# Performance work log

Measured on AMD Instinct MI355X. Metric: run time of the kernel, lower is better.

Reference implementation:

```python
import jax, jax.numpy as jnp
import numpy as np
from jax import lax

VOCAB, EMB, HID, TAGS = 8000, 300, 512, 24  # hidden_dim=512 -> 256 per direction
B, S = 128, 512
H2 = HID // 2


def setup_inputs() -> dict:
    key = jax.random.key(0)
    ks = jax.random.split(key, 16)
    sc = 0.05
    inp = {
        "chars": jax.random.randint(ks[0], (B, S), 0, VOCAB),
        "tags": jax.random.randint(ks[1], (B, S), 0, TAGS),
        "mask": jnp.ones((B, S), dtype=bool),
        "emb": jax.random.normal(ks[2], (VOCAB, EMB), jnp.float32) * sc,
        # PyTorch LSTM layout: gates stacked [i, f, g, o]
        "w_ih_f": jax.random.normal(ks[3], (4 * H2, EMB), jnp.float32) * sc,
        "w_hh_f": jax.random.normal(ks[4], (4 * H2, H2), jnp.float32) * sc,
        "b_f": jax.random.normal(ks[5], (4 * H2,), jnp.float32) * sc,  # b_ih + b_hh fused
        "w_ih_b": jax.random.normal(ks[6], (4 * H2, EMB), jnp.float32) * sc,
        "w_hh_b": jax.random.normal(ks[7], (4 * H2, H2), jnp.float32) * sc,
        "b_b": jax.random.normal(ks[8], (4 * H2,), jnp.float32) * sc,
        "w_out": jax.random.normal(ks[9], (TAGS, HID), jnp.float32) * sc,
        "b_out": jax.random.normal(ks[10], (TAGS,), jnp.float32) * sc,
        "trans": jax.random.normal(ks[11], (TAGS, TAGS), jnp.float32) * sc,
        "start_trans": jax.random.normal(ks[12], (TAGS,), jnp.float32) * sc,
        "end_trans": jax.random.normal(ks[13], (TAGS,), jnp.float32) * sc,
    }
    return inp


def _lstm_dir(x, w_ih, w_hh, b, reverse):
    # x: [B, S, E] -> h: [B, S, H2]
    gx = jnp.einsum('bse,ge->bsg', x, w_ih) + b  # [B, S, 4*H2]

    def step(carry, g_t):
        h, c = carry
        g = g_t + h @ w_hh.T
        i, f, gg, o = jnp.split(g, 4, axis=-1)
        c = jax.nn.sigmoid(f) * c + jax.nn.sigmoid(i) * jnp.tanh(gg)
        h = jax.nn.sigmoid(o) * jnp.tanh(c)
        return (h, c), h

    init = (jnp.zeros((x.shape[0], H2), x.dtype), jnp.zeros((x.shape[0], H2), x.dtype))
    _, hs = lax.scan(step, init, jnp.swapaxes(gx, 0, 1), reverse=reverse)
    return jnp.swapaxes(hs, 0, 1)


def _crf_loss(emissions, tags, mask, trans, start_trans, end_trans):
    # torchcrf log-likelihood, reduction='mean'; loss = -mean
    b, s, t = emissions.shape
    maskf = mask.astype(emissions.dtype)
    # numerator: score of gold path
    em_t = jnp.take_along_axis(emissions, tags[..., None], axis=2)[..., 0]  # [B,S]
    tr_t = trans[tags[:, :-1], tags[:, 1:]]  # [B,S-1]
    score = start_trans[tags[:, 0]] + em_t[:, 0]
    score = score + jnp.sum((em_t[:, 1:] + tr_t) * maskf[:, 1:], axis=1)
    seq_ends = jnp.sum(mask.astype(jnp.int32), axis=1) - 1  # [B]
    last_tags = jnp.take_along_axis(tags, seq_ends[:, None], axis=1)[:, 0]
    score = score + end_trans[last_tags]
    # denominator: forward algorithm via scan
    alpha0 = start_trans + emissions[:, 0]  # [B,T]

    def step(alpha, inputs):
        em, m = inputs  # em [B,T], m [B]
        nxt = jax.nn.logsumexp(alpha[:, :, None] + trans[None] + em[:, None, :], axis=1)
        alpha = jnp.where(m[:, None], nxt, alpha)
        return alpha, None

    alpha, _ = lax.scan(step, alpha0,
                        (jnp.swapaxes(emissions[:, 1:], 0, 1), jnp.swapaxes(mask[:, 1:], 0, 1)))
    log_z = jax.nn.logsumexp(alpha + end_trans, axis=1)  # [B]
    llh = score - log_z
    return -jnp.mean(llh)


def reference(chars, tags, mask, emb, w_ih_f, w_hh_f, b_f, w_ih_b, w_hh_b, b_b,
              w_out, b_out, trans, start_trans, end_trans):
    x = emb[chars]  # [B,S,E]
    h_f = _lstm_dir(x, w_ih_f, w_hh_f, b_f, reverse=False)
    h_b = _lstm_dir(x, w_ih_b, w_hh_b, b_b, reverse=True)
    lstm_out = jnp.concatenate([h_f, h_b], axis=-1)  # [B,S,HID]
    emissions = jnp.einsum('bsh,th->bst', lstm_out, w_out) + b_out  # [B,S,TAGS]
    return _crf_loss(emissions, tags, mask, trans, start_trans, end_trans)
```

## Files before the change

### kernel.cpp

```cpp
#include <hip/hip_runtime.h>
#include <math.h>

#define BB   128
#define SS   512
#define EMBD 300
#define VOC  8000
#define NTAG 24
#define BSD  (BB*SS)

#define RQI  36
#define LQQ  7

#define SW   400.0f
#define SH   512.0f
#define INVQ (1.0f / (400.0f * 512.0f))

typedef unsigned int   u32;
typedef unsigned short u16;
typedef _Float16 f16x2 __attribute__((ext_vector_type(2)));

__device__ __forceinline__ int idot4(u32 a, u32 b, int c) {
#if __has_builtin(__builtin_amdgcn_sdot4)
    return __builtin_amdgcn_sdot4((int)a, (int)b, c, false);
#elif __has_builtin(__builtin_amdgcn_sudot4)
    return __builtin_amdgcn_sudot4(true, (int)a, true, (int)b, c, false);
#else
    int s = c;
    #pragma unroll
    for (int e = 0; e < 4; ++e) {
        int xa = ((int)(a << (24 - 8 * e))) >> 24;
        int xb = ((int)(b << (24 - 8 * e))) >> 24;
        s += xa * xb;
    }
    return s;
#endif
}
__device__ __forceinline__ float sigm(float x) { return 1.0f / (1.0f + __expf(-x)); }
__device__ __forceinline__ float tanh_fast(float x) {
    return 1.0f - 2.0f / (__expf(2.0f * x) + 1.0f);
}
__device__ __forceinline__ int qclamp(float x, float s) {
    int v = (int)rintf(x * s);
    return v > 127 ? 127 : (v < -127 ? -127 : v);
}
__device__ __forceinline__ u32 q4(const float* p, float s) {
    u32 r = 0;
    #pragma unroll
    for (int e = 0; e < 4; ++e)
        r |= ((u32)(qclamp(p[e], s) & 0xFF)) << (8 * e);
    return r;
}

__global__ __launch_bounds__(512)
void k_packW(const float* __restrict__ w_hh_f, const float* __restrict__ w_hh_b,
             const float* __restrict__ w_out,
             u32* __restrict__ wregB, uint4* __restrict__ wldsB,
             u32* __restrict__ woq)
{
    const int dir = blockIdx.x;
    const int t   = threadIdx.x;
    const float* w = dir ? w_hh_b : w_hh_f;

    for (int half = 0; half < 2; ++half) {
        const int r = half * 512 + t;
        const float* row = w + (size_t)r * 256;
        for (int q = 0; q < RQI; ++q)
            wregB[((size_t)(dir * 2 + half) * RQI + q) * 512 + t] = q4(row + 4 * q, SW);
        for (int qq = 0; qq < LQQ; ++qq) {
            uint4 v;
            v.x = q4(row + 4 * (RQI + 4 * qq + 0), SW);
            v.y = q4(row + 4 * (RQI + 4 * qq + 1), SW);
            v.z = q4(row + 4 * (RQI + 4 * qq + 2), SW);
            v.w = q4(row + 4 * (RQI + 4 * qq + 3), SW);
            wldsB[((size_t)(dir * 2 + half) * LQQ + qq) * 512 + t] = v;
        }
    }
    for (int i = t; i < NTAG * 64; i += 512) {
        const int tag = i >> 6, q = i & 63;
        woq[(size_t)dir * NTAG * 64 + i] =
            q4(w_out + (size_t)tag * 512 + dir * 256 + 4 * q, SW);
    }
}

__global__ __launch_bounds__(256)
void k_gxtab(const float* __restrict__ emb,
             const float* __restrict__ w_f, const float* __restrict__ bias_f,
             const float* __restrict__ w_b, const float* __restrict__ bias_b,
             u16* __restrict__ gxtab)
{
    const int dir = blockIdx.z;
    const float* W    = dir ? w_b    : w_f;
    const float* bias = dir ? bias_b : bias_f;
    u16* out = gxtab + (size_t)dir * VOC * 1024;
    const int r0 = blockIdx.y * 64;
    const int c0 = blockIdx.x * 128;

    __shared__ float As[16][65];
    __shared__ float Bs[16][129];

    const int tid = threadIdx.x;
    const int kk = tid & 15;
    const int rr = tid >> 4;
    const int ty = tid >> 4;
    const int tx = tid & 15;

    float acc[4][8] = {};

    for (int kt = 0; kt < EMBD; kt += 16) {
        const int k = kt + kk;
        const bool kok = (k < EMBD);
        #pragma unroll
        for (int p = 0; p < 4; ++p)
            As[kk][rr + p * 16] = kok ? emb[(size_t)(r0 + rr + p * 16) * EMBD + k] : 0.0f;
        #pragma unroll
        for (int p = 0; p < 8; ++p)
            Bs[kk][rr + p * 16] = kok ? W[(size_t)(c0 + rr + p * 16) * EMBD + k] : 0.0f;
        __syncthreads();
        #pragma unroll
        for (int q = 0; q < 16; ++q) {
            float av[4], bv[8];
            #pragma unroll
            for (int i = 0; i < 4; ++i) av[i] = As[q][ty * 4 + i];
            #pragma unroll
            for (int jj = 0; jj < 8; ++jj) bv[jj] = Bs[q][jj * 16 + tx];
            #pragma unroll
            for (int i = 0; i < 4; ++i)
                #pragma unroll
                for (int jj = 0; jj < 8; ++jj)
                    acc[i][jj] = fmaf(av[i], bv[jj], acc[i][jj]);
        }
        __syncthreads();
    }

    #pragma unroll
    for (int i = 0; i < 4; ++i) {
        const size_t rb = (size_t)(r0 + ty * 4 + i) * 1024;
        #pragma unroll
        for (int jj = 0; jj < 8; ++jj) {
            const int cl = c0 + jj * 16 + tx;
            out[rb + cl] = __builtin_bit_cast(u16, (_Float16)(acc[i][jj] + bias[cl]));
        }
    }
}

__global__ __launch_bounds__(512, 2)
void k_lstm_res(const int* __restrict__ chars, const u16* __restrict__ gxtab,
                const u32* __restrict__ wregB, const uint4* __restrict__ wldsB,
                const u32* __restrict__ woq, const float* __restrict__ b_out,
                float* __restrict__ emis_f, float* __restrict__ emis_b)
{
    const int bid = blockIdx.x;
    const int dir = bid >> 7;
    const int b   = bid & 127;
    const int tid = threadIdx.x;

    __shared__ __align__(16) uint4 ldsW[2 * LQQ * 512];
    __shared__ __align__(16) u32   hq[2][64];
    __shared__ __align__(16) u32   woL[NTAG * 64];
    __shared__ __align__(16) float2 xg[256];
    __shared__ int chlds[SS];

    chlds[tid] = chars[(size_t)b * SS + tid];
    const uint4* wl = wldsB + (size_t)dir * 2 * LQQ * 512;
    #pragma unroll
    for (int q = 0; q < 2 * LQQ; ++q) ldsW[q * 512 + tid] = wl[(size_t)q * 512 + tid];
    {
        const u32* wop = woq + (size_t)dir * NTAG * 64;
        for (int i = tid; i < NTAG * 64; i += 512) woL[i] = wop[i];
    }
    if (tid < 64) hq[0][tid] = 0u;

    u32 WA[RQI], WB[RQI];
    const u32* wr = wregB + (size_t)dir * 2 * RQI * 512 + tid;
    #pragma unroll
    for (int q = 0; q < RQI; ++q) {
        WA[q] = wr[(size_t)q * 512];
        WB[q] = wr[(size_t)(RQI + q) * 512];
    }

    const u16* gxp = gxtab + (size_t)dir * VOC * 1024;
    float* emis = (dir ? emis_b : emis_f) + (size_t)b * SS * NTAG;

    const int tag = tid >> 4, part = tid & 15;
    const float bo = (tid < 384 && dir == 0) ? b_out[tag] : 0.0f;

    float c = 0.0f;
    __syncthreads();

    const int t0 = dir ? (SS - 1) : 0;
    u16 gA = gxp[(size_t)chlds[t0] * 1024 + tid];
    u16 gB = gxp[(size_t)chlds[t0] * 1024 + 512 + tid];

    int cur = 0;
    #pragma unroll 1
    for (int sloc = 0; sloc < SS; ++sloc) {
        const int t = dir ? (SS - 1 - sloc) : sloc;

        u16 gA_n = 0, gB_n = 0;
        if (sloc < SS - 1) {
            const int tn = dir ? (t - 1) : (t + 1);
            const size_t o = (size_t)chlds[tn] * 1024 + tid;
            gA_n = gxp[o];
            gB_n = gxp[o + 512];
        }

        const uint4* h16 = (const uint4*)hq[cur];
        int aA = 0, aB = 0;
        #pragma unroll
        for (int q16 = 0; q16 < 9; ++q16) {
            const uint4 hv = h16[q16];
            aA = idot4(WA[4 * q16 + 0], hv.x, aA);
            aA = idot4(WA[4 * q16 + 1], hv.y, aA);
            aA = idot4(WA[4 * q16 + 2], hv.z, aA);
            aA = idot4(WA[4 * q16 + 3], hv.w, aA);
            aB = idot4(WB[4 * q16 + 0], hv.x, aB);
            aB = idot4(WB[4 * q16 + 1], hv.y, aB);
            aB = idot4(WB[4 * q16 + 2], hv.z, aB);
            aB = idot4(WB[4 * q16 + 3], hv.w, aB);
        }
        #pragma unroll
        for (int qq = 0; qq < LQQ; ++qq) {
            const uint4 hv = h16[9 + qq];
            const uint4 wa = ldsW[qq * 512 + tid];
            const uint4 wb = ldsW[(LQQ + qq) * 512 + tid];
            aA = idot4(wa.x, hv.x, aA);
            aA = idot4(wa.y, hv.y, aA);
            aA = idot4(wa.z, hv.z, aA);
            aA = idot4(wa.w, hv.w, aA);
            aB = idot4(wb.x, hv.x, aB);
            aB = idot4(wb.y, hv.y, aB);
            aB = idot4(wb.z, hv.z, aB);
            aB = idot4(wb.w, hv.w, aB);
        }
        const float apreA = (float)aA * INVQ + (float)__builtin_bit_cast(_Float16, gA);
        const float apreB = (float)aB * INVQ + (float)__builtin_bit_cast(_Float16, gB);

        if (tid >= 256) xg[tid - 256] = make_float2(sigm(apreA), sigm(apreB));
        __syncthreads();

        if (tid < 256) {
            const float2 fo = xg[tid];
            const float ig = sigm(apreA);
            const float gg = tanh_fast(apreB);
            c = fmaf(fo.x, c, ig * gg);
            const float h = fo.y * tanh_fast(c);
            const int hi = qclamp(h, SH);
            const int b1 = __shfl_down(hi, 1);
            const int b2 = __shfl_down(hi, 2);
            const int b3 = __shfl_down(hi, 3);
            if ((tid & 3) == 0)
                hq[cur ^ 1][tid >> 2] = (u32)(hi & 0xFF) | ((u32)(b1 & 0xFF) << 8) |
                                        ((u32)(b2 & 0xFF) << 16) | ((u32)(b3 & 0xFF) << 24);
        }
        __syncthreads();

        if (tid < 384) {
            const uint4 hv = ((const uint4*)hq[cur ^ 1])[part];
            const uint4 wv = ((const uint4*)woL)[tag * 16 + part];
            int ei = idot4(wv.x, hv.x, 0);
            ei = idot4(wv.y, hv.y, ei);
            ei = idot4(wv.z, hv.z, ei);
            ei = idot4(wv.w, hv.w, ei);
            float e = (float)ei * INVQ;
            e += __shfl_down(e, 8);
            e += __shfl_down(e, 4);
            e += __shfl_down(e, 2);
            e += __shfl_down(e, 1);
            if (part == 0) emis[(size_t)t * NTAG + tag] = e + bo;
        }
        gA = gA_n; gB = gB_n;
        cur ^= 1;
    }
}

__global__ __launch_bounds__(64)
void k_crf(const float* __restrict__ emis_f, const float* __restrict__ emis_b,
           const int* __restrict__ tags,
           const float* __restrict__ trans, const float* __restrict__ start_tr,
           const float* __restrict__ end_tr, float* __restrict__ llh)
{
    const int b    = blockIdx.x;
    const int lane = threadIdx.x;
    const float* ef = emis_f + (size_t)b * SS * NTAG;
    const float* eb = emis_b + (size_t)b * SS * NTAG;
    const int*   tg = tags + (size_t)b * SS;
    const bool active = (lane < NTAG);

    float trans_reg[NTAG];
    #pragma unroll
    for (int i = 0; i < NTAG; ++i)
        trans_reg[i] = active ? trans[i * NTAG + lane] : 0.0f;

    float sc = 0.0f;
    for (int t = lane; t < SS; t += 64) {
        const int tt = tg[t];
        sc += ef[t * NTAG + tt] + eb[t * NTAG + tt];
        if (t > 0) sc += trans[tg[t - 1] * NTAG + tt];
    }
    #pragma unroll
    for (int off = 32; off > 0; off >>= 1) sc += __shfl_down(sc, off);

    float alpha = active ? (start_tr[lane] + ef[lane] + eb[lane]) : -1e30f;
    for (int t = 1; t < SS; ++t) {
        float v[NTAG];
        #pragma unroll
        for (int i = 0; i < NTAG; ++i)
            v[i] = __shfl(alpha, i) + trans_reg[i];
        float m = v[0];
        #pragma unroll
        for (int i = 1; i < NTAG; ++i) m = fmaxf(m, v[i]);
        float ssum = 0.0f;
        #pragma unroll
        for (int i = 0; i < NTAG; ++i) ssum += __expf(v[i] - m);
        const float e = active ? (ef[t * NTAG + lane] + eb[t * NTAG + lane]) : 0.0f;
        alpha = active ? (m + __logf(ssum) + e) : -1e30f;
    }

    float v = alpha + (active ? end_tr[lane] : 0.0f);
    float m = v;
    #pragma unroll
    for (int off = 32; off > 0; off >>= 1) m = fmaxf(m, __shfl_down(m, off));
    m = __shfl(m, 0);
    float e = __expf(v - m);
    #pragma unroll
    for (int off = 32; off > 0; off >>= 1) e += __shfl_down(e, off);

    if (lane == 0) {
        const float logz  = m + __logf(e);
        const float score = sc + start_tr[tg[0]] + end_tr[tg[SS - 1]];
        llh[b] = score - logz;
    }
}

__global__ __launch_bounds__(64)
void k_final(const float* __restrict__ llh, float* __restrict__ out)
{
    const int lane = threadIdx.x;
    float v = llh[lane] + llh[lane + 64];
    #pragma unroll
    for (int off = 32; off > 0; off >>= 1) v += __shfl_down(v, off);
    if (lane == 0) out[0] = -(v * (1.0f / 128.0f));
}

extern "C" void kernel_launch(void* const* d_in, const int* in_sizes, int n_in,
                              void* d_out, int out_size, void* d_ws, size_t ws_size,
                              hipStream_t stream)
{
    (void)in_sizes; (void)n_in; (void)out_size; (void)ws_size;

    const int*   chars   = (const int*)d_in[0];
    const int*   tags    = (const int*)d_in[1];
    const float* emb     = (const float*)d_in[3];
    const float* w_ih_f  = (const float*)d_in[4];
    const float* w_hh_f  = (const float*)d_in[5];
    const float* b_f     = (const float*)d_in[6];
    const float* w_ih_b  = (const float*)d_in[7];
    const float* w_hh_b  = (const float*)d_in[8];
    const float* b_b     = (const float*)d_in[9];
    const float* w_out   = (const float*)d_in[10];
    const float* b_out   = (const float*)d_in[11];
    const float* trans   = (const float*)d_in[12];
    const float* start_t = (const float*)d_in[13];
    const float* end_t   = (const float*)d_in[14];

    char* ws = (char*)d_ws;
    size_t off = 0;
    auto carve = [&](size_t bytes) -> char* {
        char* p = ws + off;
        off += (bytes + 255) & ~(size_t)255;
        return p;
    };
    u16*   gxtab  = (u16*)carve((size_t)2 * VOC * 1024 * 2);
    u32*   wregB  = (u32*)carve((size_t)2 * 2 * RQI * 512 * 4);
    uint4* wldsB  = (uint4*)carve((size_t)2 * 2 * LQQ * 512 * 16);
    u32*   woq    = (u32*)carve((size_t)2 * NTAG * 64 * 4);
    float* emis_f = (float*)carve((size_t)BSD * NTAG * 4);
    float* emis_b = (float*)carve((size_t)BSD * NTAG * 4);
    float* llh    = (float*)carve(128 * 4);

    hipLaunchKernelGGL(k_packW, dim3(2), dim3(512), 0, stream,
                       w_hh_f, w_hh_b, w_out, wregB, wldsB, woq);
    hipLaunchKernelGGL(k_gxtab, dim3(8, 125, 2), dim3(256), 0, stream,
                       emb, w_ih_f, b_f, w_ih_b, b_b, gxtab);
    hipLaunchKernelGGL(k_lstm_res, dim3(256), dim3(512), 0, stream,
                       chars, gxtab, wregB, wldsB, woq, b_out, emis_f, emis_b);
    hipLaunchKernelGGL(k_crf, dim3(128), dim3(64), 0, stream,
                       emis_f, emis_b, tags, trans, start_t, end_t, llh);
    hipLaunchKernelGGL(k_final, dim3(1), dim3(64), 0, stream,
                       llh, (float*)d_out);
}
```

Before: 1.203 ms.

## Broadcast hidden state via readlane and split recurrent weights across registers, LDS, global

The recurrent LSTM kernel now keeps the packed int8 hidden state in a per-lane register and broadcasts each word with readlane instead of reading uint4 vectors from LDS every step. The recurrent weight matrix is re-split three ways: 32 words per thread in registers (fewer than the previous 72), 14 uint4 per thread in LDS, and 10 uint4 per thread streamed from global/L2 on every timestep. The emission projection moves to the upper half of the threads, with 8 lanes per tag instead of 16. The aim is to cut VGPR pressure and LDS broadcast traffic on the serial critical path. The cost is extra global loads inside the time loop, and readlane requires the index to be wave-uniform.

```diff
diff --git a/kernel.cpp b/kernel.cpp
--- a/kernel.cpp
+++ b/kernel.cpp
@@ -8,22 +8,16 @@
 #define NTAG 24
 #define BSD  (BB*SS)
 
-#define RQI  36
-#define LQQ  7
-
 #define SW   400.0f
 #define SH   512.0f
 #define INVQ (1.0f / (400.0f * 512.0f))
 
 typedef unsigned int   u32;
 typedef unsigned short u16;
-typedef _Float16 f16x2 __attribute__((ext_vector_type(2)));
 
 __device__ __forceinline__ int idot4(u32 a, u32 b, int c) {
 #if __has_builtin(__builtin_amdgcn_sdot4)
     return __builtin_amdgcn_sdot4((int)a, (int)b, c, false);
-#elif __has_builtin(__builtin_amdgcn_sudot4)
-    return __builtin_amdgcn_sudot4(true, (int)a, true, (int)b, c, false);
 #else
     int s = c;
     #pragma unroll
@@ -35,6 +29,13 @@
     return s;
 #endif
 }
+__device__ __forceinline__ u32 rdlane(u32 v, int l) {
+#if __has_builtin(__builtin_amdgcn_readlane)
+    return (u32)__builtin_amdgcn_readlane((int)v, l);
+#else
+    return (u32)__shfl((int)v, l);
+#endif
+}
 __device__ __forceinline__ float sigm(float x) { return 1.0f / (1.0f + __expf(-x)); }
 __device__ __forceinline__ float tanh_fast(float x) {
     return 1.0f - 2.0f / (__expf(2.0f * x) + 1.0f);
@@ -54,26 +55,44 @@
 __global__ __launch_bounds__(512)
 void k_packW(const float* __restrict__ w_hh_f, const float* __restrict__ w_hh_b,
              const float* __restrict__ w_out,
-             u32* __restrict__ wregB, uint4* __restrict__ wldsB,
-             u32* __restrict__ woq)
+             u32* __restrict__ wreg, uint4* __restrict__ wlds,
+             uint4* __restrict__ wstr, u32* __restrict__ woq)
 {
     const int dir = blockIdx.x;
     const int t   = threadIdx.x;
     const float* w = dir ? w_hh_b : w_hh_f;
-
-    for (int half = 0; half < 2; ++half) {
-        const int r = half * 512 + t;
-        const float* row = w + (size_t)r * 256;
-        for (int q = 0; q < RQI; ++q)
-            wregB[((size_t)(dir * 2 + half) * RQI + q) * 512 + t] = q4(row + 4 * q, SW);
-        for (int qq = 0; qq < LQQ; ++qq) {
-            uint4 v;
-            v.x = q4(row + 4 * (RQI + 4 * qq + 0), SW);
-            v.y = q4(row + 4 * (RQI + 4 * qq + 1), SW);
-            v.z = q4(row + 4 * (RQI + 4 * qq + 2), SW);
-            v.w = q4(row + 4 * (RQI + 4 * qq + 3), SW);
-            wldsB[((size_t)(dir * 2 + half) * LQQ + qq) * 512 + t] = v;
-        }
+    const float* rowA = w + (size_t)t * 256;
+    const float* rowB = w + (size_t)(t + 512) * 256;
+
+    for (int q = 0; q < 16; ++q) {
+        wreg[((size_t)(dir * 32 + q) * 512) + t]      = q4(rowA + 4 * q, SW);
+        wreg[((size_t)(dir * 32 + 16 + q) * 512) + t] = q4(rowB + 4 * q, SW);
+    }
+    for (int qq = 0; qq < 7; ++qq) {
+        uint4 va, vb;
+        va.x = q4(rowA + 4 * (16 + 4 * qq + 0), SW);
+        va.y = q4(rowA + 4 * (16 + 4 * qq + 1), SW);
+        va.z = q4(rowA + 4 * (16 + 4 * qq + 2), SW);
+        va.w = q4(rowA + 4 * (16 + 4 * qq + 3), SW);
+        vb.x = q4(rowB + 4 * (16 + 4 * qq + 0), SW);
+        vb.y = q4(rowB + 4 * (16 + 4 * qq + 1), SW);
+        vb.z = q4(rowB + 4 * (16 + 4 * qq + 2), SW);
+        vb.w = q4(rowB + 4 * (16 + 4 * qq + 3), SW);
+        wlds[((size_t)(dir * 14 + qq) * 512) + t]     = va;
+        wlds[((size_t)(dir * 14 + 7 + qq) * 512) + t] = vb;
+    }
+    for (int qq = 0; qq < 5; ++qq) {
+        uint4 va, vb;
+        va.x = q4(rowA + 4 * (44 + 4 * qq + 0), SW);
+        va.y = q4(rowA + 4 * (44 + 4 * qq + 1), SW);
+        va.z = q4(rowA + 4 * (44 + 4 * qq + 2), SW);
+        va.w = q4(rowA + 4 * (44 + 4 * qq + 3), SW);
+        vb.x = q4(rowB + 4 * (44 + 4 * qq + 0), SW);
+        vb.y = q4(rowB + 4 * (44 + 4 * qq + 1), SW);
+        vb.z = q4(rowB + 4 * (44 + 4 * qq + 2), SW);
+        vb.w = q4(rowB + 4 * (44 + 4 * qq + 3), SW);
+        wstr[((size_t)(dir * 10 + qq) * 512) + t]     = va;
+        wstr[((size_t)(dir * 10 + 5 + qq) * 512) + t] = vb;
     }
     for (int i = t; i < NTAG * 64; i += 512) {
         const int tag = i >> 6, q = i & 63;
@@ -144,47 +163,50 @@
 }
 
 __global__ __launch_bounds__(512, 2)
-void k_lstm_res(const int* __restrict__ chars, const u16* __restrict__ gxtab,
-                const u32* __restrict__ wregB, const uint4* __restrict__ wldsB,
-                const u32* __restrict__ woq, const float* __restrict__ b_out,
-                float* __restrict__ emis_f, float* __restrict__ emis_b)
+void k_lstm_rl(const int* __restrict__ chars, const u16* __restrict__ gxtab,
+               const u32* __restrict__ wreg, const uint4* __restrict__ wlds,
+               const uint4* __restrict__ wstr, const u32* __restrict__ woq,
+               const float* __restrict__ b_out,
+               float* __restrict__ emis_f, float* __restrict__ emis_b)
 {
     const int bid = blockIdx.x;
     const int dir = bid >> 7;
     const int b   = bid & 127;
     const int tid = threadIdx.x;
 
-    __shared__ __align__(16) uint4 ldsW[2 * LQQ * 512];
+    __shared__ __align__(16) uint4 ldsW[14 * 512];
     __shared__ __align__(16) u32   hq[2][64];
     __shared__ __align__(16) u32   woL[NTAG * 64];
     __shared__ __align__(16) float2 xg[256];
     __shared__ int chlds[SS];
 
     chlds[tid] = chars[(size_t)b * SS + tid];
-    const uint4* wl = wldsB + (size_t)dir * 2 * LQQ * 512;
-    #pragma unroll
-    for (int q = 0; q < 2 * LQQ; ++q) ldsW[q * 512 + tid] = wl[(size_t)q * 512 + tid];
     {
+        const uint4* wl = wlds + (size_t)dir * 14 * 512;
+        #pragma unroll
+        for (int q = 0; q < 14; ++q) ldsW[q * 512 + tid] = wl[(size_t)q * 512 + tid];
         const u32* wop = woq + (size_t)dir * NTAG * 64;
         for (int i = tid; i < NTAG * 64; i += 512) woL[i] = wop[i];
     }
-    if (tid < 64) hq[0][tid] = 0u;
-
-    u32 WA[RQI], WB[RQI];
-    const u32* wr = wregB + (size_t)dir * 2 * RQI * 512 + tid;
-    #pragma unroll
-    for (int q = 0; q < RQI; ++q) {
-        WA[q] = wr[(size_t)q * 512];
-        WB[q] = wr[(size_t)(RQI + q) * 512];
-    }
+
+    u32 WR[32];
+    {
+        const u32* wrp = wreg + (size_t)dir * 32 * 512 + tid;
+        #pragma unroll
+        for (int q = 0; q < 32; ++q) WR[q] = wrp[(size_t)q * 512];
+    }
+    const uint4* wsp = wstr + (size_t)dir * 10 * 512 + tid;
 
     const u16* gxp = gxtab + (size_t)dir * VOC * 1024;
     float* emis = (dir ? emis_b : emis_f) + (size_t)b * SS * NTAG;
 
-    const int tag = tid >> 4, part = tid & 15;
-    const float bo = (tid < 384 && dir == 0) ? b_out[tag] : 0.0f;
+    const int etid  = tid - 256;
+    const bool edo  = (tid >= 256) && (etid < 192);
+    const int etag  = etid >> 3, epart = etid & 7;
+    const float bo  = (edo && dir == 0) ? b_out[etag] : 0.0f;
 
     float c = 0.0f;
+    u32 hreg = 0u;
     __syncthreads();
 
     const int t0 = dir ? (SS - 1) : 0;
@@ -203,34 +225,42 @@
             gA_n = gxp[o];
             gB_n = gxp[o + 512];
         }
-
-        const uint4* h16 = (const uint4*)hq[cur];
+        uint4 s[10];
+        #pragma unroll
+        for (int qq = 0; qq < 10; ++qq) s[qq] = wsp[(size_t)qq * 512];
+
         int aA = 0, aB = 0;
         #pragma unroll
-        for (int q16 = 0; q16 < 9; ++q16) {
-            const uint4 hv = h16[q16];
-            aA = idot4(WA[4 * q16 + 0], hv.x, aA);
-            aA = idot4(WA[4 * q16 + 1], hv.y, aA);
-            aA = idot4(WA[4 * q16 + 2], hv.z, aA);
-            aA = idot4(WA[4 * q16 + 3], hv.w, aA);
-            aB = idot4(WB[4 * q16 + 0], hv.x, aB);
-            aB = idot4(WB[4 * q16 + 1], hv.y, aB);
-            aB = idot4(WB[4 * q16 + 2], hv.z, aB);
-            aB = idot4(WB[4 * q16 + 3], hv.w, aB);
-        }
-        #pragma unroll
-        for (int qq = 0; qq < LQQ; ++qq) {
-            const uint4 hv = h16[9 + qq];
+        for (int q = 0; q < 16; ++q) {
+            const u32 hs = rdlane(hreg, q);
+            aA = idot4(WR[q], hs, aA);
+            aB = idot4(WR[16 + q], hs, aB);
+        }
+        #pragma unroll
+        for (int qq = 0; qq < 7; ++qq) {
             const uint4 wa = ldsW[qq * 512 + tid];
-            const uint4 wb = ldsW[(LQQ + qq) * 512 + tid];
-            aA = idot4(wa.x, hv.x, aA);
-            aA = idot4(wa.y, hv.y, aA);
-            aA = idot4(wa.z, hv.z, aA);
-            aA = idot4(wa.w, hv.w, aA);
-            aB = idot4(wb.x, hv.x, aB);
-            aB = idot4(wb.y, hv.y, aB);
-            aB = idot4(wb.z, hv.z, aB);
-            aB = idot4(wb.w, hv.w, aB);
+            const uint4 wb = ldsW[(7 + qq) * 512 + tid];
+            const u32 h0 = rdlane(hreg, 16 + 4 * qq + 0);
+            const u32 h1 = rdlane(hreg, 16 + 4 * qq + 1);
+            const u32 h2 = rdlane(hreg, 16 + 4 * qq + 2);
+            const u32 h3 = rdlane(hreg, 16 + 4 * qq + 3);
+            aA = idot4(wa.x, h0, aA); aB = idot4(wb.x, h0, aB);
+            aA = idot4(wa.y, h1, aA); aB = idot4(wb.y, h1, aB);
+            aA = idot4(wa.z, h2, aA); aB = idot4(wb.z, h2, aB);
+            aA = idot4(wa.w, h3, aA); aB = idot4(wb.w, h3, aB);
+        }
+        #pragma unroll
+        for (int qq = 0; qq < 5; ++qq) {
+            const uint4 wa = s[qq];
+            const uint4 wb = s[5 + qq];
+            const u32 h0 = rdlane(hreg, 44 + 4 * qq + 0);
+            const u32 h1 = rdlane(hreg, 44 + 4 * qq + 1);
+            const u32 h2 = rdlane(hreg, 44 + 4 * qq + 2);
+            const u32 h3 = rdlane(hreg, 44 + 4 * qq + 3);
+            aA = idot4(wa.x, h0, aA); aB = idot4(wb.x, h0, aB);
+            aA = idot4(wa.y, h1, aA); aB = idot4(wb.y, h1, aB);
+            aA = idot4(wa.z, h2, aA); aB = idot4(wb.z, h2, aB);
+            aA = idot4(wa.w, h3, aA); aB = idot4(wb.w, h3, aB);
         }
         const float apreA = (float)aA * INVQ + (float)__builtin_bit_cast(_Float16, gA);
         const float apreB = (float)aB * INVQ + (float)__builtin_bit_cast(_Float16, gB);
@@ -254,19 +284,27 @@
         }
         __syncthreads();
 
-        if (tid < 384) {
-            const uint4 hv = ((const uint4*)hq[cur ^ 1])[part];
-            const uint4 wv = ((const uint4*)woL)[tag * 16 + part];
-            int ei = idot4(wv.x, hv.x, 0);
-            ei = idot4(wv.y, hv.y, ei);
-            ei = idot4(wv.z, hv.z, ei);
-            ei = idot4(wv.w, hv.w, ei);
+        hreg = hq[cur ^ 1][tid & 63];
+
+        if (edo) {
+            const uint4* hn4 = (const uint4*)hq[cur ^ 1];
+            const uint4* wp  = (const uint4*)woL;
+            const uint4 h0 = hn4[epart * 2], h1 = hn4[epart * 2 + 1];
+            const uint4 w0 = wp[etag * 16 + epart * 2];
+            const uint4 w1 = wp[etag * 16 + epart * 2 + 1];
+            int ei = idot4(w0.x, h0.x, 0);
+            ei = idot4(w0.y, h0.y, ei);
+            ei = idot4(w0.z, h0.z, ei);
+            ei = idot4(w0.w, h0.w, ei);
+            ei = idot4(w1.x, h1.x, ei);
+            ei = idot4(w1.y, h1.y, ei);
+            ei = idot4(w1.z, h1.z, ei);
+            ei = idot4(w1.w, h1.w, ei);
             float e = (float)ei * INVQ;
-            e += __shfl_down(e, 8);
             e += __shfl_down(e, 4);
             e += __shfl_down(e, 2);
             e += __shfl_down(e, 1);
-            if (part == 0) emis[(size_t)t * NTAG + tag] = e + bo;
+            if (epart == 0) emis[(size_t)t * NTAG + etag] = e + bo;
         }
         gA = gA_n; gB = gB_n;
         cur ^= 1;
@@ -371,19 +409,20 @@
         return p;
     };
     u16*   gxtab  = (u16*)carve((size_t)2 * VOC * 1024 * 2);
-    u32*   wregB  = (u32*)carve((size_t)2 * 2 * RQI * 512 * 4);
-    uint4* wldsB  = (uint4*)carve((size_t)2 * 2 * LQQ * 512 * 16);
+    u32*   wreg   = (u32*)carve((size_t)2 * 32 * 512 * 4);
+    uint4* wlds   = (uint4*)carve((size_t)2 * 14 * 512 * 16);
+    uint4* wstr   = (uint4*)carve((size_t)2 * 10 * 512 * 16);
     u32*   woq    = (u32*)carve((size_t)2 * NTAG * 64 * 4);
     float* emis_f = (float*)carve((size_t)BSD * NTAG * 4);
     float* emis_b = (float*)carve((size_t)BSD * NTAG * 4);
     float* llh    = (float*)carve(128 * 4);
 
     hipLaunchKernelGGL(k_packW, dim3(2), dim3(512), 0, stream,
-                       w_hh_f, w_hh_b, w_out, wregB, wldsB, woq);
+                       w_hh_f, w_hh_b, w_out, wreg, wlds, wstr, woq);
     hipLaunchKernelGGL(k_gxtab, dim3(8, 125, 2), dim3(256), 0, stream,
                        emb, w_ih_f, b_f, w_ih_b, b_b, gxtab);
-    hipLaunchKernelGGL(k_lstm_res, dim3(256), dim3(512), 0, stream,
-                       chars, gxtab, wregB, wldsB, woq, b_out, emis_f, emis_b);
+    hipLaunchKernelGGL(k_lstm_rl, dim3(256), dim3(512), 0, stream,
+                       chars, gxtab, wreg, wlds, wstr, woq, b_out, emis_f, emis_b);
     hipLaunchKernelGGL(k_crf, dim3(128), dim3(64), 0, stream,
                        emis_f, emis_b, tags, trans, start_t, end_t, llh);
     hipLaunchKernelGGL(k_final, dim3(1), dim3(64), 0, stream,
```

Result: faster. 1.179 ms, median of 2 (-2.0%).
